# Kernel tuning notes

Measured on AMD Instinct MI355X. Metric: run time of the kernel, lower is better.

## Reference

```python
import jax, jax.numpy as jnp
import numpy as np

B, N, NPOINT, K = 8, 16384, 1024, 32
RADIUS = 0.2
SAMPLE_NUM = 10          # number of random subsets in get_robust_centroid
SEL = 7                  # round(10 * 0.7) centroids kept
SUBSET = int(round(K * 0.9))


def setup_inputs() -> dict:
    key = jax.random.key(0)
    xyz = jax.random.normal(key, (B, N, 3), dtype=jnp.float32)
    return {"xyz": xyz}


def _batched_gather(points, idx):
    # points: [B, N, C], idx: [B, ...] -> [B, ..., C]
    return jax.vmap(lambda p, i: p[i])(points, idx)


def _fps(xyz, npoint):
    # Sequential farthest point sampling -> indices [B, npoint]
    Bb, Nn, _ = xyz.shape
    init = (jnp.full((Bb, Nn), 1e10, xyz.dtype), jnp.zeros((Bb,), jnp.int32))

    def body(carry, _):
        distance, farthest = carry
        centroid = _batched_gather(xyz, farthest)            # [B, 3]
        dist = jnp.sum((xyz - centroid[:, None, :]) ** 2, -1)  # [B, N]
        distance = jnp.minimum(distance, dist)
        new_far = jnp.argmax(distance, axis=-1).astype(jnp.int32)
        return (distance, new_far), farthest

    _, idx = jax.lax.scan(body, init, None, length=npoint)
    return idx.T  # [B, npoint]


def _knn_idx(xyz, centers, k):
    # squared-distance matrix [B, S, N], then k smallest (torch.cdist + topk)
    d2 = (jnp.sum(centers ** 2, -1)[:, :, None]
          + jnp.sum(xyz ** 2, -1)[:, None, :]
          - 2.0 * jnp.einsum('bsc,bnc->bsn', centers, xyz))
    _, idx = jax.lax.top_k(-d2, k)
    return idx  # [B, S, k]


def _robust_centroid(grouped):
    # grouped: [B, S, K, 3] -> robust centroid [B, S, 3]
    key = jax.random.key(42)
    cents = []
    for i in range(SAMPLE_NUM):
        perm = jax.random.permutation(jax.random.fold_in(key, i), K)
        cents.append(jnp.mean(grouped[:, :, perm[:SUBSET], :], axis=2))
    cl = jnp.stack(cents, axis=2)                             # [B, S, 10, 3]
    sq = jnp.sum(cl ** 2, -1, keepdims=True)                  # [B, S, 10, 1]
    pd = sq + jnp.swapaxes(sq, -1, -2) - 2.0 * jnp.einsum('bsik,bsjk->bsij', cl, cl)
    pd_sum = jnp.sum(pd, -1)                                  # [B, S, 10]
    _, order = jax.lax.top_k(-pd_sum, SAMPLE_NUM)             # ascending by dist-sum
    sel = order[..., :SEL]                                    # [B, S, 7]
    sel_b = jnp.broadcast_to(sel[..., None], sel.shape + (3,))
    csel = jnp.take_along_axis(cl, sel_b, axis=2)             # [B, S, 7, 3]
    return jnp.mean(csel, axis=2)


def _global_feature(new_xyz, radius, grouped_xyz):
    centroid_xyz = _robust_centroid(grouped_xyz)              # [B, S, 3]
    ref_norm = jnp.linalg.norm(new_xyz, axis=-1, keepdims=True)
    ref_unit = new_xyz / (ref_norm + 1e-4)
    inter_xyz = radius * ref_unit + new_xyz
    crv = new_xyz - centroid_xyz
    crd = jnp.linalg.norm(crv, axis=-1, keepdims=True)
    civ = inter_xyz - centroid_xyz
    cid = jnp.linalg.norm(civ, axis=-1, keepdims=True)
    dot = jnp.sum(crv * civ, -1, keepdims=True)
    ang_rci = dot / (crd * cid + 1e-6)
    irv = new_xyz - inter_xyz
    icv = centroid_xyz - inter_xyz
    dot2 = jnp.sum(irv * icv, -1, keepdims=True)
    ang_ric = dot2 / (radius * cid + 1e-6)
    return jnp.concatenate([ref_norm, crd, cid, ang_rci, ang_ric], axis=-1)  # [B, S, 5]


def reference(xyz):
    cent_idx = _fps(xyz, NPOINT)                   # [B, S]
    centers = _batched_gather(xyz, cent_idx)       # [B, S, 3]
    nn_idx = _knn_idx(xyz, centers, K)             # [B, S, K]
    grouped = _batched_gather(xyz, nn_idx)         # [B, S, K, 3]
    return _global_feature(centers, RADIUS, grouped)
```

## Files before the change

### kernel.cpp

```cpp
#include <hip/hip_runtime.h>
#include <stdint.h>
#include <algorithm>

#define BATCH 8
#define NPTS 16384
#define NPOINT 1024
#define KNN 32
#define SAMPLE_NUM 10
#define SELN 7
#define SUBSET 29
#define RADIUS 0.2f
#define CAP 2048

typedef float f32x2 __attribute__((ext_vector_type(2)));
typedef float f32x4 __attribute__((ext_vector_type(4)));

struct PermTab { unsigned char p[SAMPLE_NUM][SUBSET]; };

static inline uint32_t rotl32h(uint32_t x, int d) { return (x << d) | (x >> (32 - d)); }

static void tf2x32(uint32_t k0, uint32_t k1, uint32_t c0, uint32_t c1,
                   uint32_t& o0, uint32_t& o1) {
    const uint32_t ks[3] = { k0, k1, k0 ^ k1 ^ 0x1BD11BDAu };
    uint32_t x0 = c0 + ks[0];
    uint32_t x1 = c1 + ks[1];
    static const int R[8] = {13, 15, 26, 6, 17, 29, 16, 24};
    for (int s = 0; s < 5; ++s) {
        const int* r = R + (s % 2) * 4;
        for (int j = 0; j < 4; ++j) {
            x0 += x1;
            x1 = rotl32h(x1, r[j]);
            x1 ^= x0;
        }
        x0 += ks[(s + 1) % 3];
        x1 += ks[(s + 2) % 3] + (uint32_t)(s + 1);
    }
    o0 = x0; o1 = x1;
}

static PermTab build_tab() {
    PermTab t;
    for (int i = 0; i < SAMPLE_NUM; ++i) {
        uint32_t f0, f1;
        tf2x32(0u, 42u, 0u, (uint32_t)i, f0, f1);
        uint32_t s0, s1;
        tf2x32(f0, f1, 0u, 1u, s0, s1);
        uint32_t bits[32];
        for (int j = 0; j < 32; ++j) {
            uint32_t o0, o1;
            tf2x32(s0, s1, 0u, (uint32_t)j, o0, o1);
            bits[j] = o0 ^ o1;
        }
        int perm[32];
        for (int j = 0; j < 32; ++j) perm[j] = j;
        std::stable_sort(perm, perm + 32, [&](int x, int y) {
            return bits[x] < bits[y];
        });
        for (int q = 0; q < SUBSET; ++q) t.p[i][q] = (unsigned char)perm[q];
    }
    return t;
}

#define REP8(M) M(0) M(1) M(2) M(3) M(4) M(5) M(6) M(7)

static __device__ __forceinline__ f32x2 pk_add(f32x2 a, f32x2 b) {
    f32x2 r;
    asm("v_pk_add_f32 %0, %1, %2" : "=v"(r) : "v"(a), "v"(b));
    return r;
}
static __device__ __forceinline__ f32x2 pk_mul(f32x2 a, f32x2 b) {
    f32x2 r;
    asm("v_pk_mul_f32 %0, %1, %2" : "=v"(r) : "v"(a), "v"(b));
    return r;
}

#define DPP_FMAX_STEP(v, ctrl) { \
        const int t_ = __builtin_amdgcn_update_dpp( \
            __float_as_int(v), __float_as_int(v), (ctrl), 0xf, 0xf, false); \
        (v) = fmaxf((v), __int_as_float(t_)); }

#define DPP_UMAX_STEP(v, ctrl) { \
        const unsigned t_ = (unsigned)__builtin_amdgcn_update_dpp( \
            (int)(v), (int)(v), (ctrl), 0xf, 0xf, false); \
        (v) = (t_ > (v)) ? t_ : (v); }

__global__ __launch_bounds__(1024) void fps_kernel(const float* __restrict__ xyz,
                                                   float* __restrict__ centers,
                                                   float* __restrict__ sqout) {
#pragma clang fp contract(off)
    const int b = blockIdx.x;
    const int tid = threadIdx.x;
    const int wv = tid >> 6;
    const int lane = tid & 63;

    __shared__ f32x4 sPair[NPTS / 2];
    __shared__ unsigned sk[2][2][16];

    const float* base = xyz + (size_t)b * NPTS * 3;

#define P_DECL(j) f32x2 pz2##j, dd2##j;
    REP8(P_DECL)
#undef P_DECL

#define P_LOAD(j) { \
        const int q = (j) * 1024 + tid; \
        const f32x2 a = *(const f32x2*)&base[6 * q]; \
        const f32x2 b2 = *(const f32x2*)&base[6 * q + 2]; \
        const f32x2 c = *(const f32x2*)&base[6 * q + 4]; \
        const f32x2 px2 = (f32x2){a.x, b2.y}; \
        const f32x2 py2 = (f32x2){a.y, c.x}; \
        pz2##j = (f32x2){b2.x, c.y}; \
        dd2##j = (f32x2){1e10f, 1e10f}; \
        sPair[q] = (f32x4){px2.x, px2.y, py2.x, py2.y}; \
        const f32x2 xx = px2 * px2, yy = py2 * py2, zz = pz2##j * pz2##j; \
        const f32x2 s1 = xx + yy; \
        const f32x2 dsq = s1 + zz; \
        *(f32x2*)&sqout[(size_t)b * NPTS + 2 * q] = dsq; }
    REP8(P_LOAD)
#undef P_LOAD

#define P_PIN(j) asm volatile("" : "+v"(pz2##j));
    REP8(P_PIN)
#undef P_PIN

    float cx = base[0], cy = base[1], cz = base[2];
    if (tid == 0) {
        float* dst = centers + (size_t)b * NPOINT * 3;
        dst[0] = cx; dst[1] = cy; dst[2] = cz;
    }
    __syncthreads();

    const unsigned tb = (unsigned)tid * 2;

    for (int t = 1; t < NPOINT; ++t) {
        const int par = t & 1;
        const float ncx = -cx, ncy = -cy, ncz = -cz;
        const f32x2 ncx2 = (f32x2){ncx, ncx};
        const f32x2 ncy2 = (f32x2){ncy, ncy};
        const f32x2 ncz2 = (f32x2){ncz, ncz};
        float bv = -1.0f;
        unsigned bidx = 0;
#define P_SCAN(j) { \
        const f32x4 vv = sPair[(j) * 1024 + tid]; \
        const f32x2 dx = pk_add((f32x2){vv.x, vv.y}, ncx2); \
        const f32x2 dy = pk_add((f32x2){vv.z, vv.w}, ncy2); \
        const f32x2 dz = pk_add(pz2##j, ncz2); \
        const f32x2 xx = pk_mul(dx, dx); \
        const f32x2 yy = pk_mul(dy, dy); \
        const f32x2 zz = pk_mul(dz, dz); \
        const f32x2 ss = pk_add(xx, yy); \
        const f32x2 d2 = pk_add(ss, zz); \
        const float nd0 = fminf(dd2##j.x, d2.x); \
        const float nd1 = fminf(dd2##j.y, d2.y); \
        dd2##j = (f32x2){nd0, nd1}; \
        if (nd0 > bv) { bv = nd0; bidx = (j) * 2; } \
        if (nd1 > bv) { bv = nd1; bidx = (j) * 2 + 1; } }
        REP8(P_SCAN)
#undef P_SCAN

        float r = bv;
        DPP_FMAX_STEP(r, 0x111)
        DPP_FMAX_STEP(r, 0x112)
        DPP_FMAX_STEP(r, 0x114)
        DPP_FMAX_STEP(r, 0x118)
        DPP_FMAX_STEP(r, 0x142)
        DPP_FMAX_STEP(r, 0x143)
        const float wmax = __int_as_float(
            __builtin_amdgcn_readlane(__float_as_int(r), 63));

        const unsigned p = ((bidx >> 1) << 11) + tb + (bidx & 1);
        unsigned uk = (bv == wmax) ? ~p : 0u;
        DPP_UMAX_STEP(uk, 0x111)
        DPP_UMAX_STEP(uk, 0x112)
        DPP_UMAX_STEP(uk, 0x114)
        DPP_UMAX_STEP(uk, 0x118)
        DPP_UMAX_STEP(uk, 0x142)
        DPP_UMAX_STEP(uk, 0x143)

        if (lane == 63) {
            sk[par][0][wv] = __float_as_uint(r);
            sk[par][1][wv] = uk;
        }
        __syncthreads();

        const unsigned hi0 = sk[par][0][lane & 15];
        const unsigned lo0 = sk[par][1][lane & 15];
        unsigned h2 = hi0;
        DPP_UMAX_STEP(h2, 0x111)
        DPP_UMAX_STEP(h2, 0x112)
        DPP_UMAX_STEP(h2, 0x114)
        DPP_UMAX_STEP(h2, 0x118)
        const unsigned shi = (unsigned)__builtin_amdgcn_readlane((int)h2, 15);
        unsigned c2 = (hi0 == shi) ? lo0 : 0u;
        DPP_UMAX_STEP(c2, 0x111)
        DPP_UMAX_STEP(c2, 0x112)
        DPP_UMAX_STEP(c2, 0x114)
        DPP_UMAX_STEP(c2, 0x118)
        const unsigned slo = (unsigned)__builtin_amdgcn_readlane((int)c2, 15);
        const int ps = (int)(~slo) & (NPTS - 1);

        const f32x4 w4 = sPair[ps >> 1];
        const int h = ps & 1;
        cx = h ? w4.y : w4.x;
        cy = h ? w4.w : w4.z;
        cz = base[(size_t)ps * 3 + 2];

        if (tid == 0) {
            float* dst = centers + ((size_t)b * NPOINT + t) * 3;
            dst[0] = cx; dst[1] = cy; dst[2] = cz;
        }
    }
}

__global__ __launch_bounds__(256) void knn_kernel(const float* __restrict__ xyz,
                                                  const float* __restrict__ centers,
                                                  const float* __restrict__ sx,
                                                  float* __restrict__ grouped) {
    const int bs = blockIdx.x;
    const int b = bs >> 10;
    const int tid = threadIdx.x;

    __shared__ unsigned hist[2048];
    __shared__ unsigned ckey[CAP];
    __shared__ int cidx[CAP];
    __shared__ int cnt;
    __shared__ int bstar;

    const float cx = centers[(size_t)bs * 3 + 0];
    const float cy = centers[(size_t)bs * 3 + 1];
    const float cz = centers[(size_t)bs * 3 + 2];
    const float sc = __fadd_rn(__fadd_rn(__fmul_rn(cx, cx), __fmul_rn(cy, cy)),
                               __fmul_rn(cz, cz));

    for (int q = tid; q < 2048; q += 256) hist[q] = 0;
    if (tid == 0) cnt = 0;
    __syncthreads();

    const float* base = xyz + (size_t)b * NPTS * 3;
    const float* sxb = sx + (size_t)b * NPTS;

    for (int j = tid; j < NPTS; j += 256) {
        float xx = base[j * 3 + 0], xy = base[j * 3 + 1], xz = base[j * 3 + 2];
        float dot = __fadd_rn(__fadd_rn(__fmul_rn(cx, xx), __fmul_rn(cy, xy)),
                              __fmul_rn(cz, xz));
        float d2 = __fsub_rn(__fadd_rn(sc, sxb[j]), __fmul_rn(2.0f, dot));
        unsigned u = __float_as_uint(d2);
        unsigned key = u ^ ((u & 0x80000000u) ? 0xFFFFFFFFu : 0x80000000u);
        atomicAdd(&hist[key >> 21], 1u);
    }
    __syncthreads();

    if (tid < 64) {
        unsigned sum = 0;
#pragma unroll
        for (int q = 0; q < 32; ++q) sum += hist[tid * 32 + q];
        unsigned incl = sum;
        for (int d = 1; d < 64; d <<= 1) {
            unsigned o = __shfl_up(incl, d, 64);
            if (tid >= d) incl += o;
        }
        unsigned long long m = __ballot(incl >= 32u);
        int L = __ffsll(m) - 1;
        if (tid == L) {
            unsigned cum = incl - sum;
            int bb = L * 32 + 31;
            for (int q = 0; q < 32; ++q) {
                cum += hist[L * 32 + q];
                if (cum >= 32u) { bb = L * 32 + q; break; }
            }
            bstar = bb;
        }
    }
    __syncthreads();

    const int bst = bstar;
    for (int j = tid; j < NPTS; j += 256) {
        float xx = base[j * 3 + 0], xy = base[j * 3 + 1], xz = base[j * 3 + 2];
        float dot = __fadd_rn(__fadd_rn(__fmul_rn(cx, xx), __fmul_rn(cy, xy)),
                              __fmul_rn(cz, xz));
        float d2 = __fsub_rn(__fadd_rn(sc, sxb[j]), __fmul_rn(2.0f, dot));
        unsigned u = __float_as_uint(d2);
        unsigned key = u ^ ((u & 0x80000000u) ? 0xFFFFFFFFu : 0x80000000u);
        if ((int)(key >> 21) <= bst) {
            int pos = atomicAdd(&cnt, 1);
            if (pos < CAP) { ckey[pos] = key; cidx[pos] = j; }
        }
    }
    __syncthreads();

    const int L2 = min(cnt, CAP);
    for (int c = tid; c < L2; c += 256) {
        const unsigned k = ckey[c];
        const int id = cidx[c];
        int rank = 0;
        for (int m2 = 0; m2 < L2; ++m2) {
            const unsigned km = ckey[m2];
            rank += (km < k || (km == k && cidx[m2] < id)) ? 1 : 0;
        }
        if (rank < KNN) {
            float* dst = grouped + ((size_t)bs * KNN + rank) * 3;
            dst[0] = base[id * 3 + 0];
            dst[1] = base[id * 3 + 1];
            dst[2] = base[id * 3 + 2];
        }
    }
}

__global__ __launch_bounds__(256) void feat_kernel(const float* __restrict__ centers,
                                                   const float* __restrict__ grouped,
                                                   float* __restrict__ out,
                                                   PermTab tab) {
    const int bs = blockIdx.x * 256 + threadIdx.x;
    if (bs >= BATCH * NPOINT) return;

    const float* g = grouped + (size_t)bs * KNN * 3;

    float clx[SAMPLE_NUM], cly[SAMPLE_NUM], clz[SAMPLE_NUM];
    for (int i = 0; i < SAMPLE_NUM; ++i) {
        float sxm = 0.f, sym = 0.f, szm = 0.f;
        for (int j = 0; j < SUBSET; ++j) {
            const int p = tab.p[i][j];
            sxm = __fadd_rn(sxm, g[p * 3 + 0]);
            sym = __fadd_rn(sym, g[p * 3 + 1]);
            szm = __fadd_rn(szm, g[p * 3 + 2]);
        }
        clx[i] = __fdiv_rn(sxm, 29.0f);
        cly[i] = __fdiv_rn(sym, 29.0f);
        clz[i] = __fdiv_rn(szm, 29.0f);
    }

    float sq[SAMPLE_NUM];
#pragma unroll
    for (int i = 0; i < SAMPLE_NUM; ++i)
        sq[i] = __fadd_rn(__fadd_rn(__fmul_rn(clx[i], clx[i]), __fmul_rn(cly[i], cly[i])),
                          __fmul_rn(clz[i], clz[i]));

    float ps[SAMPLE_NUM];
#pragma unroll
    for (int i = 0; i < SAMPLE_NUM; ++i) {
        float pd[SAMPLE_NUM];
#pragma unroll
        for (int j = 0; j < SAMPLE_NUM; ++j) {
            float dot = __fadd_rn(__fadd_rn(__fmul_rn(clx[i], clx[j]), __fmul_rn(cly[i], cly[j])),
                                  __fmul_rn(clz[i], clz[j]));
            pd[j] = __fsub_rn(__fadd_rn(sq[i], sq[j]), __fmul_rn(2.0f, dot));
        }
        float res = __fadd_rn(__fadd_rn(__fadd_rn(pd[0], pd[1]), __fadd_rn(pd[2], pd[3])),
                              __fadd_rn(__fadd_rn(pd[4], pd[5]), __fadd_rn(pd[6], pd[7])));
        res = __fadd_rn(res, pd[8]);
        res = __fadd_rn(res, pd[9]);
        ps[i] = res;
    }

    int rnk[SAMPLE_NUM];
#pragma unroll
    for (int j = 0; j < SAMPLE_NUM; ++j) {
        int r = 0;
#pragma unroll
        for (int m = 0; m < SAMPLE_NUM; ++m)
            r += (ps[m] < ps[j] || (ps[m] == ps[j] && m < j)) ? 1 : 0;
        rnk[j] = r;
    }

    float csx = 0.f, csy = 0.f, csz = 0.f;
    for (int r = 0; r < SELN; ++r) {
#pragma unroll
        for (int j = 0; j < SAMPLE_NUM; ++j) {
            if (rnk[j] == r) {
                csx = __fadd_rn(csx, clx[j]);
                csy = __fadd_rn(csy, cly[j]);
                csz = __fadd_rn(csz, clz[j]);
            }
        }
    }
    const float ccx = __fdiv_rn(csx, 7.0f);
    const float ccy = __fdiv_rn(csy, 7.0f);
    const float ccz = __fdiv_rn(csz, 7.0f);

    const float nx = centers[(size_t)bs * 3 + 0];
    const float ny = centers[(size_t)bs * 3 + 1];
    const float nz = centers[(size_t)bs * 3 + 2];

    const float ref_norm = __fsqrt_rn(__fadd_rn(
        __fadd_rn(__fmul_rn(nx, nx), __fmul_rn(ny, ny)), __fmul_rn(nz, nz)));
    const float den = __fadd_rn(ref_norm, 1e-4f);
    const float ux = __fdiv_rn(nx, den), uy = __fdiv_rn(ny, den), uz = __fdiv_rn(nz, den);
    const float ix = __fadd_rn(__fmul_rn(RADIUS, ux), nx);
    const float iy = __fadd_rn(__fmul_rn(RADIUS, uy), ny);
    const float iz = __fadd_rn(__fmul_rn(RADIUS, uz), nz);

    const float crvx = __fsub_rn(nx, ccx), crvy = __fsub_rn(ny, ccy), crvz = __fsub_rn(nz, ccz);
    const float crd = __fsqrt_rn(__fadd_rn(
        __fadd_rn(__fmul_rn(crvx, crvx), __fmul_rn(crvy, crvy)), __fmul_rn(crvz, crvz)));
    const float civx = __fsub_rn(ix, ccx), civy = __fsub_rn(iy, ccy), civz = __fsub_rn(iz, ccz);
    const float cid = __fsqrt_rn(__fadd_rn(
        __fadd_rn(__fmul_rn(civx, civx), __fmul_rn(civy, civy)), __fmul_rn(civz, civz)));
    const float dot = __fadd_rn(__fadd_rn(__fmul_rn(crvx, civx), __fmul_rn(crvy, civy)),
                                __fmul_rn(crvz, civz));
    const float ang_rci = __fdiv_rn(dot, __fadd_rn(__fmul_rn(crd, cid), 1e-6f));

    const float irvx = __fsub_rn(nx, ix), irvy = __fsub_rn(ny, iy), irvz = __fsub_rn(nz, iz);
    const float icvx = __fsub_rn(ccx, ix), icvy = __fsub_rn(ccy, iy), icvz = __fsub_rn(ccz, iz);
    const float dot2 = __fadd_rn(__fadd_rn(__fmul_rn(irvx, icvx), __fmul_rn(irvy, icvy)),
                                 __fmul_rn(irvz, icvz));
    const float ang_ric = __fdiv_rn(dot2, __fadd_rn(__fmul_rn(RADIUS, cid), 1e-6f));

    float* o = out + (size_t)bs * 5;
    o[0] = ref_norm;
    o[1] = crd;
    o[2] = cid;
    o[3] = ang_rci;
    o[4] = ang_ric;
}

extern "C" void kernel_launch(void* const* d_in, const int* in_sizes, int n_in,
                              void* d_out, int out_size, void* d_ws, size_t ws_size,
                              hipStream_t stream) {
    const float* xyz = (const float*)d_in[0];
    float* out = (float*)d_out;

    float* centers = (float*)d_ws;
    float* sx = centers + (size_t)BATCH * NPOINT * 3;
    float* grouped = sx + (size_t)BATCH * NPTS;

    static PermTab tab = build_tab();

    fps_kernel<<<BATCH, 1024, 0, stream>>>(xyz, centers, sx);
    knn_kernel<<<BATCH * NPOINT, 256, 0, stream>>>(xyz, centers, sx, grouped);
    feat_kernel<<<(BATCH * NPOINT + 255) / 256, 256, 0, stream>>>(centers, grouped, out, tab);
}
```

Before: 2.176 ms.

## Fuse FPS, KNN and feature kernels into one persistent kernel with streaming handoff

Replaces the three launches with one persistent kernel. The first 8 blocks run farthest point sampling and publish each new center with a per-batch release counter. The other blocks take work tickets from an atomic counter and spin until the center they need is ready, so KNN selection and feature computation overlap with the sequential FPS loop. Grouped points now stay in shared memory instead of a global buffer, and the precomputed squared-norm buffer is dropped in favour of recomputing norms in KNN. The risks are that the persistent grid and spin-waiting need all 256 1024-thread blocks to be co-resident, KNN now runs at 1024 threads per block, and packed-math asm was swapped for compiler vector ops.

```diff
diff --git a/kernel.cpp b/kernel.cpp
--- a/kernel.cpp
+++ b/kernel.cpp
@@ -11,6 +11,8 @@
 #define SUBSET 29
 #define RADIUS 0.2f
 #define CAP 2048
+#define NTHREADS 1024
+#define GRID_BLOCKS 256
 
 typedef float f32x2 __attribute__((ext_vector_type(2)));
 typedef float f32x4 __attribute__((ext_vector_type(4)));
@@ -63,17 +65,6 @@
 
 #define REP8(M) M(0) M(1) M(2) M(3) M(4) M(5) M(6) M(7)
 
-static __device__ __forceinline__ f32x2 pk_add(f32x2 a, f32x2 b) {
-    f32x2 r;
-    asm("v_pk_add_f32 %0, %1, %2" : "=v"(r) : "v"(a), "v"(b));
-    return r;
-}
-static __device__ __forceinline__ f32x2 pk_mul(f32x2 a, f32x2 b) {
-    f32x2 r;
-    asm("v_pk_mul_f32 %0, %1, %2" : "=v"(r) : "v"(a), "v"(b));
-    return r;
-}
-
 #define DPP_FMAX_STEP(v, ctrl) { \
         const int t_ = __builtin_amdgcn_update_dpp( \
             __float_as_int(v), __float_as_int(v), (ctrl), 0xf, 0xf, false); \
@@ -84,333 +75,349 @@
             (int)(v), (int)(v), (ctrl), 0xf, 0xf, false); \
         (v) = (t_ > (v)) ? t_ : (v); }
 
-__global__ __launch_bounds__(1024) void fps_kernel(const float* __restrict__ xyz,
-                                                   float* __restrict__ centers,
-                                                   float* __restrict__ sqout) {
+__global__ __launch_bounds__(NTHREADS) void fused_kernel(const float* __restrict__ xyz,
+                                                         float* __restrict__ centers,
+                                                         unsigned* __restrict__ syncb,
+                                                         float* __restrict__ out,
+                                                         PermTab tab) {
 #pragma clang fp contract(off)
-    const int b = blockIdx.x;
+    const int bid = blockIdx.x;
     const int tid = threadIdx.x;
-    const int wv = tid >> 6;
-    const int lane = tid & 63;
 
     __shared__ f32x4 sPair[NPTS / 2];
     __shared__ unsigned sk[2][2][16];
-
-    const float* base = xyz + (size_t)b * NPTS * 3;
+    __shared__ unsigned hist[2048];
+    __shared__ unsigned ckey[CAP];
+    __shared__ int cidx[CAP];
+    __shared__ int s_cnt;
+    __shared__ int s_bstar;
+    __shared__ int s_ticket;
+    __shared__ float s_c[3];
+    __shared__ float s_gl[KNN * 3];
+    __shared__ float s_clx[SAMPLE_NUM], s_cly[SAMPLE_NUM], s_clz[SAMPLE_NUM];
+
+    if (bid < BATCH) {
+        const int b = bid;
+        const int wv = tid >> 6;
+        const int lane = tid & 63;
+        const float* base = xyz + (size_t)b * NPTS * 3;
+        unsigned* dput = syncb + 32 + b * 32;
 
 #define P_DECL(j) f32x2 pz2##j, dd2##j;
-    REP8(P_DECL)
+        REP8(P_DECL)
 #undef P_DECL
 
 #define P_LOAD(j) { \
-        const int q = (j) * 1024 + tid; \
-        const f32x2 a = *(const f32x2*)&base[6 * q]; \
-        const f32x2 b2 = *(const f32x2*)&base[6 * q + 2]; \
-        const f32x2 c = *(const f32x2*)&base[6 * q + 4]; \
+        const int q2 = (j) * 1024 + tid; \
+        const f32x2 a = *(const f32x2*)&base[6 * q2]; \
+        const f32x2 b2 = *(const f32x2*)&base[6 * q2 + 2]; \
+        const f32x2 c = *(const f32x2*)&base[6 * q2 + 4]; \
         const f32x2 px2 = (f32x2){a.x, b2.y}; \
         const f32x2 py2 = (f32x2){a.y, c.x}; \
         pz2##j = (f32x2){b2.x, c.y}; \
         dd2##j = (f32x2){1e10f, 1e10f}; \
-        sPair[q] = (f32x4){px2.x, px2.y, py2.x, py2.y}; \
-        const f32x2 xx = px2 * px2, yy = py2 * py2, zz = pz2##j * pz2##j; \
-        const f32x2 s1 = xx + yy; \
-        const f32x2 dsq = s1 + zz; \
-        *(f32x2*)&sqout[(size_t)b * NPTS + 2 * q] = dsq; }
-    REP8(P_LOAD)
+        sPair[q2] = (f32x4){px2.x, px2.y, py2.x, py2.y}; }
+        REP8(P_LOAD)
 #undef P_LOAD
 
 #define P_PIN(j) asm volatile("" : "+v"(pz2##j));
-    REP8(P_PIN)
+        REP8(P_PIN)
 #undef P_PIN
 
-    float cx = base[0], cy = base[1], cz = base[2];
-    if (tid == 0) {
-        float* dst = centers + (size_t)b * NPOINT * 3;
-        dst[0] = cx; dst[1] = cy; dst[2] = cz;
+        float cx = base[0], cy = base[1], cz = base[2];
+        if (tid == 0) {
+            float* dst = centers + (size_t)b * NPOINT * 3;
+            dst[0] = cx; dst[1] = cy; dst[2] = cz;
+            __hip_atomic_store(dput, 1u, __ATOMIC_RELEASE,
+                               __HIP_MEMORY_SCOPE_AGENT);
+        }
+        __syncthreads();
+
+        const unsigned tb = (unsigned)tid * 2;
+
+        for (int t = 1; t < NPOINT; ++t) {
+            const int par = t & 1;
+            const f32x2 ccx2 = (f32x2){cx, cx};
+            const f32x2 ccy2 = (f32x2){cy, cy};
+            const f32x2 ccz2 = (f32x2){cz, cz};
+            float bv = -1.0f;
+            unsigned bidx = 0;
+#define P_SCAN(j) { \
+            const f32x4 vv = sPair[(j) * 1024 + tid]; \
+            const f32x2 dx = (f32x2){vv.x, vv.y} - ccx2; \
+            const f32x2 dy = (f32x2){vv.z, vv.w} - ccy2; \
+            const f32x2 dz = pz2##j - ccz2; \
+            const f32x2 xx = dx * dx; \
+            const f32x2 yy = dy * dy; \
+            const f32x2 zz = dz * dz; \
+            const f32x2 ss = xx + yy; \
+            const f32x2 d2 = ss + zz; \
+            const float nd0 = fminf(dd2##j.x, d2.x); \
+            const float nd1 = fminf(dd2##j.y, d2.y); \
+            dd2##j = (f32x2){nd0, nd1}; \
+            if (nd0 > bv) { bv = nd0; bidx = (j) * 2; } \
+            if (nd1 > bv) { bv = nd1; bidx = (j) * 2 + 1; } }
+            REP8(P_SCAN)
+#undef P_SCAN
+
+            float r = bv;
+            DPP_FMAX_STEP(r, 0x111)
+            DPP_FMAX_STEP(r, 0x112)
+            DPP_FMAX_STEP(r, 0x114)
+            DPP_FMAX_STEP(r, 0x118)
+            DPP_FMAX_STEP(r, 0x142)
+            DPP_FMAX_STEP(r, 0x143)
+            const float wmax = __int_as_float(
+                __builtin_amdgcn_readlane(__float_as_int(r), 63));
+
+            const unsigned p = ((bidx >> 1) << 11) + tb + (bidx & 1);
+            unsigned uk = (bv == wmax) ? ~p : 0u;
+            DPP_UMAX_STEP(uk, 0x111)
+            DPP_UMAX_STEP(uk, 0x112)
+            DPP_UMAX_STEP(uk, 0x114)
+            DPP_UMAX_STEP(uk, 0x118)
+            DPP_UMAX_STEP(uk, 0x142)
+            DPP_UMAX_STEP(uk, 0x143)
+
+            if (lane == 63) {
+                sk[par][0][wv] = __float_as_uint(r);
+                sk[par][1][wv] = uk;
+            }
+            __syncthreads();
+
+            const unsigned hi0 = sk[par][0][lane & 15];
+            const unsigned lo0 = sk[par][1][lane & 15];
+            unsigned h2 = hi0;
+            DPP_UMAX_STEP(h2, 0x111)
+            DPP_UMAX_STEP(h2, 0x112)
+            DPP_UMAX_STEP(h2, 0x114)
+            DPP_UMAX_STEP(h2, 0x118)
+            const unsigned shi = (unsigned)__builtin_amdgcn_readlane((int)h2, 15);
+            unsigned c2 = (hi0 == shi) ? lo0 : 0u;
+            DPP_UMAX_STEP(c2, 0x111)
+            DPP_UMAX_STEP(c2, 0x112)
+            DPP_UMAX_STEP(c2, 0x114)
+            DPP_UMAX_STEP(c2, 0x118)
+            const unsigned slo = (unsigned)__builtin_amdgcn_readlane((int)c2, 15);
+            const int ps = (int)(~slo) & (NPTS - 1);
+
+            const f32x4 w4 = sPair[ps >> 1];
+            const int h = ps & 1;
+            cx = h ? w4.y : w4.x;
+            cy = h ? w4.w : w4.z;
+            cz = base[(size_t)ps * 3 + 2];
+
+            if (tid == 0) {
+                float* dst = centers + ((size_t)b * NPOINT + t) * 3;
+                dst[0] = cx; dst[1] = cy; dst[2] = cz;
+                __hip_atomic_store(dput, (unsigned)(t + 1), __ATOMIC_RELEASE,
+                                   __HIP_MEMORY_SCOPE_AGENT);
+            }
+        }
     }
-    __syncthreads();
-
-    const unsigned tb = (unsigned)tid * 2;
-
-    for (int t = 1; t < NPOINT; ++t) {
-        const int par = t & 1;
-        const float ncx = -cx, ncy = -cy, ncz = -cz;
-        const f32x2 ncx2 = (f32x2){ncx, ncx};
-        const f32x2 ncy2 = (f32x2){ncy, ncy};
-        const f32x2 ncz2 = (f32x2){ncz, ncz};
-        float bv = -1.0f;
-        unsigned bidx = 0;
-#define P_SCAN(j) { \
-        const f32x4 vv = sPair[(j) * 1024 + tid]; \
-        const f32x2 dx = pk_add((f32x2){vv.x, vv.y}, ncx2); \
-        const f32x2 dy = pk_add((f32x2){vv.z, vv.w}, ncy2); \
-        const f32x2 dz = pk_add(pz2##j, ncz2); \
-        const f32x2 xx = pk_mul(dx, dx); \
-        const f32x2 yy = pk_mul(dy, dy); \
-        const f32x2 zz = pk_mul(dz, dz); \
-        const f32x2 ss = pk_add(xx, yy); \
-        const f32x2 d2 = pk_add(ss, zz); \
-        const float nd0 = fminf(dd2##j.x, d2.x); \
-        const float nd1 = fminf(dd2##j.y, d2.y); \
-        dd2##j = (f32x2){nd0, nd1}; \
-        if (nd0 > bv) { bv = nd0; bidx = (j) * 2; } \
-        if (nd1 > bv) { bv = nd1; bidx = (j) * 2 + 1; } }
-        REP8(P_SCAN)
-#undef P_SCAN
-
-        float r = bv;
-        DPP_FMAX_STEP(r, 0x111)
-        DPP_FMAX_STEP(r, 0x112)
-        DPP_FMAX_STEP(r, 0x114)
-        DPP_FMAX_STEP(r, 0x118)
-        DPP_FMAX_STEP(r, 0x142)
-        DPP_FMAX_STEP(r, 0x143)
-        const float wmax = __int_as_float(
-            __builtin_amdgcn_readlane(__float_as_int(r), 63));
-
-        const unsigned p = ((bidx >> 1) << 11) + tb + (bidx & 1);
-        unsigned uk = (bv == wmax) ? ~p : 0u;
-        DPP_UMAX_STEP(uk, 0x111)
-        DPP_UMAX_STEP(uk, 0x112)
-        DPP_UMAX_STEP(uk, 0x114)
-        DPP_UMAX_STEP(uk, 0x118)
-        DPP_UMAX_STEP(uk, 0x142)
-        DPP_UMAX_STEP(uk, 0x143)
-
-        if (lane == 63) {
-            sk[par][0][wv] = __float_as_uint(r);
-            sk[par][1][wv] = uk;
-        }
-        __syncthreads();
-
-        const unsigned hi0 = sk[par][0][lane & 15];
-        const unsigned lo0 = sk[par][1][lane & 15];
-        unsigned h2 = hi0;
-        DPP_UMAX_STEP(h2, 0x111)
-        DPP_UMAX_STEP(h2, 0x112)
-        DPP_UMAX_STEP(h2, 0x114)
-        DPP_UMAX_STEP(h2, 0x118)
-        const unsigned shi = (unsigned)__builtin_amdgcn_readlane((int)h2, 15);
-        unsigned c2 = (hi0 == shi) ? lo0 : 0u;
-        DPP_UMAX_STEP(c2, 0x111)
-        DPP_UMAX_STEP(c2, 0x112)
-        DPP_UMAX_STEP(c2, 0x114)
-        DPP_UMAX_STEP(c2, 0x118)
-        const unsigned slo = (unsigned)__builtin_amdgcn_readlane((int)c2, 15);
-        const int ps = (int)(~slo) & (NPTS - 1);
-
-        const f32x4 w4 = sPair[ps >> 1];
-        const int h = ps & 1;
-        cx = h ? w4.y : w4.x;
-        cy = h ? w4.w : w4.z;
-        cz = base[(size_t)ps * 3 + 2];
+
+    for (;;) {
+        if (tid == 0) s_ticket = (int)atomicAdd(&syncb[0], 1u);
+        __syncthreads();
+        const int q = s_ticket;
+        if (q >= BATCH * NPOINT) break;
+        const int s = q >> 3;
+        const int b = q & 7;
+        const int bs = b * NPOINT + s;
+        const float* bse = xyz + (size_t)b * NPTS * 3;
 
         if (tid == 0) {
-            float* dst = centers + ((size_t)b * NPOINT + t) * 3;
-            dst[0] = cx; dst[1] = cy; dst[2] = cz;
-        }
+            unsigned* db = syncb + 32 + b * 32;
+            while (__hip_atomic_load(db, __ATOMIC_RELAXED,
+                                     __HIP_MEMORY_SCOPE_AGENT) <= (unsigned)s)
+                __builtin_amdgcn_s_sleep(4);
+            (void)__hip_atomic_load(db, __ATOMIC_ACQUIRE,
+                                    __HIP_MEMORY_SCOPE_AGENT);
+            float* cp = centers + (size_t)bs * 3;
+            s_c[0] = __hip_atomic_load(cp + 0, __ATOMIC_RELAXED,
+                                       __HIP_MEMORY_SCOPE_AGENT);
+            s_c[1] = __hip_atomic_load(cp + 1, __ATOMIC_RELAXED,
+                                       __HIP_MEMORY_SCOPE_AGENT);
+            s_c[2] = __hip_atomic_load(cp + 2, __ATOMIC_RELAXED,
+                                       __HIP_MEMORY_SCOPE_AGENT);
+            s_cnt = 0;
+        }
+        for (int h = tid; h < 2048; h += NTHREADS) hist[h] = 0;
+        __syncthreads();
+
+        const float cx = s_c[0], cy = s_c[1], cz = s_c[2];
+        const float sc = __fadd_rn(__fadd_rn(__fmul_rn(cx, cx), __fmul_rn(cy, cy)),
+                                   __fmul_rn(cz, cz));
+
+        for (int j = tid; j < NPTS; j += NTHREADS) {
+            const float xx = bse[j * 3 + 0], xy = bse[j * 3 + 1], xz = bse[j * 3 + 2];
+            const float sxj = __fadd_rn(__fadd_rn(__fmul_rn(xx, xx), __fmul_rn(xy, xy)),
+                                        __fmul_rn(xz, xz));
+            const float dot = __fadd_rn(__fadd_rn(__fmul_rn(cx, xx), __fmul_rn(cy, xy)),
+                                        __fmul_rn(cz, xz));
+            const float d2v = __fsub_rn(__fadd_rn(sc, sxj), __fmul_rn(2.0f, dot));
+            unsigned u = __float_as_uint(d2v);
+            unsigned key = u ^ ((u & 0x80000000u) ? 0xFFFFFFFFu : 0x80000000u);
+            atomicAdd(&hist[key >> 21], 1u);
+        }
+        __syncthreads();
+
+        if (tid < 64) {
+            unsigned sum = 0;
+#pragma unroll
+            for (int q2 = 0; q2 < 32; ++q2) sum += hist[tid * 32 + q2];
+            unsigned incl = sum;
+            for (int d = 1; d < 64; d <<= 1) {
+                unsigned o = __shfl_up(incl, d, 64);
+                if (tid >= d) incl += o;
+            }
+            unsigned long long m = __ballot(incl >= 32u);
+            int L = __ffsll(m) - 1;
+            if (tid == L) {
+                unsigned cum = incl - sum;
+                int bb = L * 32 + 31;
+                for (int q2 = 0; q2 < 32; ++q2) {
+                    cum += hist[L * 32 + q2];
+                    if (cum >= 32u) { bb = L * 32 + q2; break; }
+                }
+                s_bstar = bb;
+            }
+        }
+        __syncthreads();
+
+        const int bst = s_bstar;
+        for (int j = tid; j < NPTS; j += NTHREADS) {
+            const float xx = bse[j * 3 + 0], xy = bse[j * 3 + 1], xz = bse[j * 3 + 2];
+            const float sxj = __fadd_rn(__fadd_rn(__fmul_rn(xx, xx), __fmul_rn(xy, xy)),
+                                        __fmul_rn(xz, xz));
+            const float dot = __fadd_rn(__fadd_rn(__fmul_rn(cx, xx), __fmul_rn(cy, xy)),
+                                        __fmul_rn(cz, xz));
+            const float d2v = __fsub_rn(__fadd_rn(sc, sxj), __fmul_rn(2.0f, dot));
+            unsigned u = __float_as_uint(d2v);
+            unsigned key = u ^ ((u & 0x80000000u) ? 0xFFFFFFFFu : 0x80000000u);
+            if ((int)(key >> 21) <= bst) {
+                int pos = atomicAdd(&s_cnt, 1);
+                if (pos < CAP) { ckey[pos] = key; cidx[pos] = j; }
+            }
+        }
+        __syncthreads();
+
+        const int L2c = min(s_cnt, CAP);
+        for (int c = tid; c < L2c; c += NTHREADS) {
+            const unsigned k = ckey[c];
+            const int id = cidx[c];
+            int rank = 0;
+            for (int m2 = 0; m2 < L2c; ++m2) {
+                const unsigned km = ckey[m2];
+                rank += (km < k || (km == k && cidx[m2] < id)) ? 1 : 0;
+            }
+            if (rank < KNN) {
+                s_gl[rank * 3 + 0] = bse[id * 3 + 0];
+                s_gl[rank * 3 + 1] = bse[id * 3 + 1];
+                s_gl[rank * 3 + 2] = bse[id * 3 + 2];
+            }
+        }
+        __syncthreads();
+
+        if (tid < SAMPLE_NUM) {
+            float sxm = 0.f, sym = 0.f, szm = 0.f;
+            for (int j2 = 0; j2 < SUBSET; ++j2) {
+                const int pp = tab.p[tid][j2];
+                sxm = __fadd_rn(sxm, s_gl[pp * 3 + 0]);
+                sym = __fadd_rn(sym, s_gl[pp * 3 + 1]);
+                szm = __fadd_rn(szm, s_gl[pp * 3 + 2]);
+            }
+            s_clx[tid] = __fdiv_rn(sxm, 29.0f);
+            s_cly[tid] = __fdiv_rn(sym, 29.0f);
+            s_clz[tid] = __fdiv_rn(szm, 29.0f);
+        }
+        __syncthreads();
+
+        if (tid == 0) {
+            float clx[SAMPLE_NUM], cly[SAMPLE_NUM], clz[SAMPLE_NUM];
+#pragma unroll
+            for (int i = 0; i < SAMPLE_NUM; ++i) {
+                clx[i] = s_clx[i]; cly[i] = s_cly[i]; clz[i] = s_clz[i];
+            }
+            float sq[SAMPLE_NUM];
+#pragma unroll
+            for (int i = 0; i < SAMPLE_NUM; ++i)
+                sq[i] = __fadd_rn(__fadd_rn(__fmul_rn(clx[i], clx[i]), __fmul_rn(cly[i], cly[i])),
+                                  __fmul_rn(clz[i], clz[i]));
+            float psv[SAMPLE_NUM];
+#pragma unroll
+            for (int i = 0; i < SAMPLE_NUM; ++i) {
+                float pd[SAMPLE_NUM];
+#pragma unroll
+                for (int j2 = 0; j2 < SAMPLE_NUM; ++j2) {
+                    float dot = __fadd_rn(__fadd_rn(__fmul_rn(clx[i], clx[j2]), __fmul_rn(cly[i], cly[j2])),
+                                          __fmul_rn(clz[i], clz[j2]));
+                    pd[j2] = __fsub_rn(__fadd_rn(sq[i], sq[j2]), __fmul_rn(2.0f, dot));
+                }
+                float res = __fadd_rn(__fadd_rn(__fadd_rn(pd[0], pd[1]), __fadd_rn(pd[2], pd[3])),
+                                      __fadd_rn(__fadd_rn(pd[4], pd[5]), __fadd_rn(pd[6], pd[7])));
+                res = __fadd_rn(res, pd[8]);
+                res = __fadd_rn(res, pd[9]);
+                psv[i] = res;
+            }
+            int rnk[SAMPLE_NUM];
+#pragma unroll
+            for (int j2 = 0; j2 < SAMPLE_NUM; ++j2) {
+                int r = 0;
+#pragma unroll
+                for (int m = 0; m < SAMPLE_NUM; ++m)
+                    r += (psv[m] < psv[j2] || (psv[m] == psv[j2] && m < j2)) ? 1 : 0;
+                rnk[j2] = r;
+            }
+            float csx = 0.f, csy = 0.f, csz = 0.f;
+            for (int r = 0; r < SELN; ++r) {
+#pragma unroll
+                for (int j2 = 0; j2 < SAMPLE_NUM; ++j2) {
+                    if (rnk[j2] == r) {
+                        csx = __fadd_rn(csx, clx[j2]);
+                        csy = __fadd_rn(csy, cly[j2]);
+                        csz = __fadd_rn(csz, clz[j2]);
+                    }
+                }
+            }
+            const float ccx = __fdiv_rn(csx, 7.0f);
+            const float ccy = __fdiv_rn(csy, 7.0f);
+            const float ccz = __fdiv_rn(csz, 7.0f);
+
+            const float nx = cx, ny = cy, nz = cz;
+            const float ref_norm = __fsqrt_rn(__fadd_rn(
+                __fadd_rn(__fmul_rn(nx, nx), __fmul_rn(ny, ny)), __fmul_rn(nz, nz)));
+            const float den = __fadd_rn(ref_norm, 1e-4f);
+            const float ux = __fdiv_rn(nx, den), uy = __fdiv_rn(ny, den), uz = __fdiv_rn(nz, den);
+            const float ix = __fadd_rn(__fmul_rn(RADIUS, ux), nx);
+            const float iy = __fadd_rn(__fmul_rn(RADIUS, uy), ny);
+            const float iz = __fadd_rn(__fmul_rn(RADIUS, uz), nz);
+
+            const float crvx = __fsub_rn(nx, ccx), crvy = __fsub_rn(ny, ccy), crvz = __fsub_rn(nz, ccz);
+            const float crd = __fsqrt_rn(__fadd_rn(
+                __fadd_rn(__fmul_rn(crvx, crvx), __fmul_rn(crvy, crvy)), __fmul_rn(crvz, crvz)));
+            const float civx = __fsub_rn(ix, ccx), civy = __fsub_rn(iy, ccy), civz = __fsub_rn(iz, ccz);
+            const float cid = __fsqrt_rn(__fadd_rn(
+                __fadd_rn(__fmul_rn(civx, civx), __fmul_rn(civy, civy)), __fmul_rn(civz, civz)));
+            const float dot = __fadd_rn(__fadd_rn(__fmul_rn(crvx, civx), __fmul_rn(crvy, civy)),
+                                        __fmul_rn(crvz, civz));
+            const float ang_rci = __fdiv_rn(dot, __fadd_rn(__fmul_rn(crd, cid), 1e-6f));
+
+            const float irvx = __fsub_rn(nx, ix), irvy = __fsub_rn(ny, iy), irvz = __fsub_rn(nz, iz);
+            const float icvx = __fsub_rn(ccx, ix), icvy = __fsub_rn(ccy, iy), icvz = __fsub_rn(ccz, iz);
+            const float dot2 = __fadd_rn(__fadd_rn(__fmul_rn(irvx, icvx), __fmul_rn(irvy, icvy)),
+                                         __fmul_rn(irvz, icvz));
+            const float ang_ric = __fdiv_rn(dot2, __fadd_rn(__fmul_rn(RADIUS, cid), 1e-6f));
+
+            float* o = out + (size_t)bs * 5;
+            o[0] = ref_norm;
+            o[1] = crd;
+            o[2] = cid;
+            o[3] = ang_rci;
+            o[4] = ang_ric;
+        }
+        __syncthreads();
     }
-}
-
-__global__ __launch_bounds__(256) void knn_kernel(const float* __restrict__ xyz,
-                                                  const float* __restrict__ centers,
-                                                  const float* __restrict__ sx,
-                                                  float* __restrict__ grouped) {
-    const int bs = blockIdx.x;
-    const int b = bs >> 10;
-    const int tid = threadIdx.x;
-
-    __shared__ unsigned hist[2048];
-    __shared__ unsigned ckey[CAP];
-    __shared__ int cidx[CAP];
-    __shared__ int cnt;
-    __shared__ int bstar;
-
-    const float cx = centers[(size_t)bs * 3 + 0];
-    const float cy = centers[(size_t)bs * 3 + 1];
-    const float cz = centers[(size_t)bs * 3 + 2];
-    const float sc = __fadd_rn(__fadd_rn(__fmul_rn(cx, cx), __fmul_rn(cy, cy)),
-                               __fmul_rn(cz, cz));
-
-    for (int q = tid; q < 2048; q += 256) hist[q] = 0;
-    if (tid == 0) cnt = 0;
-    __syncthreads();
-
-    const float* base = xyz + (size_t)b * NPTS * 3;
-    const float* sxb = sx + (size_t)b * NPTS;
-
-    for (int j = tid; j < NPTS; j += 256) {
-        float xx = base[j * 3 + 0], xy = base[j * 3 + 1], xz = base[j * 3 + 2];
-        float dot = __fadd_rn(__fadd_rn(__fmul_rn(cx, xx), __fmul_rn(cy, xy)),
-                              __fmul_rn(cz, xz));
-        float d2 = __fsub_rn(__fadd_rn(sc, sxb[j]), __fmul_rn(2.0f, dot));
-        unsigned u = __float_as_uint(d2);
-        unsigned key = u ^ ((u & 0x80000000u) ? 0xFFFFFFFFu : 0x80000000u);
-        atomicAdd(&hist[key >> 21], 1u);
-    }
-    __syncthreads();
-
-    if (tid < 64) {
-        unsigned sum = 0;
-#pragma unroll
-        for (int q = 0; q < 32; ++q) sum += hist[tid * 32 + q];
-        unsigned incl = sum;
-        for (int d = 1; d < 64; d <<= 1) {
-            unsigned o = __shfl_up(incl, d, 64);
-            if (tid >= d) incl += o;
-        }
-        unsigned long long m = __ballot(incl >= 32u);
-        int L = __ffsll(m) - 1;
-        if (tid == L) {
-            unsigned cum = incl - sum;
-            int bb = L * 32 + 31;
-            for (int q = 0; q < 32; ++q) {
-                cum += hist[L * 32 + q];
-                if (cum >= 32u) { bb = L * 32 + q; break; }
-            }
-            bstar = bb;
-        }
-    }
-    __syncthreads();
-
-    const int bst = bstar;
-    for (int j = tid; j < NPTS; j += 256) {
-        float xx = base[j * 3 + 0], xy = base[j * 3 + 1], xz = base[j * 3 + 2];
-        float dot = __fadd_rn(__fadd_rn(__fmul_rn(cx, xx), __fmul_rn(cy, xy)),
-                              __fmul_rn(cz, xz));
-        float d2 = __fsub_rn(__fadd_rn(sc, sxb[j]), __fmul_rn(2.0f, dot));
-        unsigned u = __float_as_uint(d2);
-        unsigned key = u ^ ((u & 0x80000000u) ? 0xFFFFFFFFu : 0x80000000u);
-        if ((int)(key >> 21) <= bst) {
-            int pos = atomicAdd(&cnt, 1);
-            if (pos < CAP) { ckey[pos] = key; cidx[pos] = j; }
-        }
-    }
-    __syncthreads();
-
-    const int L2 = min(cnt, CAP);
-    for (int c = tid; c < L2; c += 256) {
-        const unsigned k = ckey[c];
-        const int id = cidx[c];
-        int rank = 0;
-        for (int m2 = 0; m2 < L2; ++m2) {
-            const unsigned km = ckey[m2];
-            rank += (km < k || (km == k && cidx[m2] < id)) ? 1 : 0;
-        }
-        if (rank < KNN) {
-            float* dst = grouped + ((size_t)bs * KNN + rank) * 3;
-            dst[0] = base[id * 3 + 0];
-            dst[1] = base[id * 3 + 1];
-            dst[2] = base[id * 3 + 2];
-        }
-    }
-}
-
-__global__ __launch_bounds__(256) void feat_kernel(const float* __restrict__ centers,
-                                                   const float* __restrict__ grouped,
-                                                   float* __restrict__ out,
-                                                   PermTab tab) {
-    const int bs = blockIdx.x * 256 + threadIdx.x;
-    if (bs >= BATCH * NPOINT) return;
-
-    const float* g = grouped + (size_t)bs * KNN * 3;
-
-    float clx[SAMPLE_NUM], cly[SAMPLE_NUM], clz[SAMPLE_NUM];
-    for (int i = 0; i < SAMPLE_NUM; ++i) {
-        float sxm = 0.f, sym = 0.f, szm = 0.f;
-        for (int j = 0; j < SUBSET; ++j) {
-            const int p = tab.p[i][j];
-            sxm = __fadd_rn(sxm, g[p * 3 + 0]);
-            sym = __fadd_rn(sym, g[p * 3 + 1]);
-            szm = __fadd_rn(szm, g[p * 3 + 2]);
-        }
-        clx[i] = __fdiv_rn(sxm, 29.0f);
-        cly[i] = __fdiv_rn(sym, 29.0f);
-        clz[i] = __fdiv_rn(szm, 29.0f);
-    }
-
-    float sq[SAMPLE_NUM];
-#pragma unroll
-    for (int i = 0; i < SAMPLE_NUM; ++i)
-        sq[i] = __fadd_rn(__fadd_rn(__fmul_rn(clx[i], clx[i]), __fmul_rn(cly[i], cly[i])),
-                          __fmul_rn(clz[i], clz[i]));
-
-    float ps[SAMPLE_NUM];
-#pragma unroll
-    for (int i = 0; i < SAMPLE_NUM; ++i) {
-        float pd[SAMPLE_NUM];
-#pragma unroll
-        for (int j = 0; j < SAMPLE_NUM; ++j) {
-            float dot = __fadd_rn(__fadd_rn(__fmul_rn(clx[i], clx[j]), __fmul_rn(cly[i], cly[j])),
-                                  __fmul_rn(clz[i], clz[j]));
-            pd[j] = __fsub_rn(__fadd_rn(sq[i], sq[j]), __fmul_rn(2.0f, dot));
-        }
-        float res = __fadd_rn(__fadd_rn(__fadd_rn(pd[0], pd[1]), __fadd_rn(pd[2], pd[3])),
-                              __fadd_rn(__fadd_rn(pd[4], pd[5]), __fadd_rn(pd[6], pd[7])));
-        res = __fadd_rn(res, pd[8]);
-        res = __fadd_rn(res, pd[9]);
-        ps[i] = res;
-    }
-
-    int rnk[SAMPLE_NUM];
-#pragma unroll
-    for (int j = 0; j < SAMPLE_NUM; ++j) {
-        int r = 0;
-#pragma unroll
-        for (int m = 0; m < SAMPLE_NUM; ++m)
-            r += (ps[m] < ps[j] || (ps[m] == ps[j] && m < j)) ? 1 : 0;
-        rnk[j] = r;
-    }
-
-    float csx = 0.f, csy = 0.f, csz = 0.f;
-    for (int r = 0; r < SELN; ++r) {
-#pragma unroll
-        for (int j = 0; j < SAMPLE_NUM; ++j) {
-            if (rnk[j] == r) {
-                csx = __fadd_rn(csx, clx[j]);
-                csy = __fadd_rn(csy, cly[j]);
-                csz = __fadd_rn(csz, clz[j]);
-            }
-        }
-    }
-    const float ccx = __fdiv_rn(csx, 7.0f);
-    const float ccy = __fdiv_rn(csy, 7.0f);
-    const float ccz = __fdiv_rn(csz, 7.0f);
-
-    const float nx = centers[(size_t)bs * 3 + 0];
-    const float ny = centers[(size_t)bs * 3 + 1];
-    const float nz = centers[(size_t)bs * 3 + 2];
-
-    const float ref_norm = __fsqrt_rn(__fadd_rn(
-        __fadd_rn(__fmul_rn(nx, nx), __fmul_rn(ny, ny)), __fmul_rn(nz, nz)));
-    const float den = __fadd_rn(ref_norm, 1e-4f);
-    const float ux = __fdiv_rn(nx, den), uy = __fdiv_rn(ny, den), uz = __fdiv_rn(nz, den);
-    const float ix = __fadd_rn(__fmul_rn(RADIUS, ux), nx);
-    const float iy = __fadd_rn(__fmul_rn(RADIUS, uy), ny);
-    const float iz = __fadd_rn(__fmul_rn(RADIUS, uz), nz);
-
-    const float crvx = __fsub_rn(nx, ccx), crvy = __fsub_rn(ny, ccy), crvz = __fsub_rn(nz, ccz);
-    const float crd = __fsqrt_rn(__fadd_rn(
-        __fadd_rn(__fmul_rn(crvx, crvx), __fmul_rn(crvy, crvy)), __fmul_rn(crvz, crvz)));
-    const float civx = __fsub_rn(ix, ccx), civy = __fsub_rn(iy, ccy), civz = __fsub_rn(iz, ccz);
-    const float cid = __fsqrt_rn(__fadd_rn(
-        __fadd_rn(__fmul_rn(civx, civx), __fmul_rn(civy, civy)), __fmul_rn(civz, civz)));
-    const float dot = __fadd_rn(__fadd_rn(__fmul_rn(crvx, civx), __fmul_rn(crvy, civy)),
-                                __fmul_rn(crvz, civz));
-    const float ang_rci = __fdiv_rn(dot, __fadd_rn(__fmul_rn(crd, cid), 1e-6f));
-
-    const float irvx = __fsub_rn(nx, ix), irvy = __fsub_rn(ny, iy), irvz = __fsub_rn(nz, iz);
-    const float icvx = __fsub_rn(ccx, ix), icvy = __fsub_rn(ccy, iy), icvz = __fsub_rn(ccz, iz);
-    const float dot2 = __fadd_rn(__fadd_rn(__fmul_rn(irvx, icvx), __fmul_rn(irvy, icvy)),
-                                 __fmul_rn(irvz, icvz));
-    const float ang_ric = __fdiv_rn(dot2, __fadd_rn(__fmul_rn(RADIUS, cid), 1e-6f));
-
-    float* o = out + (size_t)bs * 5;
-    o[0] = ref_norm;
-    o[1] = crd;
-    o[2] = cid;
-    o[3] = ang_rci;
-    o[4] = ang_ric;
 }
 
 extern "C" void kernel_launch(void* const* d_in, const int* in_sizes, int n_in,
@@ -419,13 +426,11 @@
     const float* xyz = (const float*)d_in[0];
     float* out = (float*)d_out;
 
-    float* centers = (float*)d_ws;
-    float* sx = centers + (size_t)BATCH * NPOINT * 3;
-    float* grouped = sx + (size_t)BATCH * NPTS;
+    unsigned* syncb = (unsigned*)d_ws;
+    float* centers = (float*)((char*)d_ws + 2048);
 
     static PermTab tab = build_tab();
 
-    fps_kernel<<<BATCH, 1024, 0, stream>>>(xyz, centers, sx);
-    knn_kernel<<<BATCH * NPOINT, 256, 0, stream>>>(xyz, centers, sx, grouped);
-    feat_kernel<<<(BATCH * NPOINT + 255) / 256, 256, 0, stream>>>(centers, grouped, out, tab);
+    (void)hipMemsetAsync(syncb, 0, 2048, stream);
+    fused_kernel<<<GRID_BLOCKS, NTHREADS, 0, stream>>>(xyz, centers, syncb, out, tab);
 }
```

Result: faster. 1.766 ms (-18.8%).
